# Kernel tuning notes

Hardware: AMD Instinct MI355X
Metric: run time of the kernel (lower is better)

## Reference

```python
import jax, jax.numpy as jnp
import numpy as np

B, N, D, H = 128, 32768, 768, 16
DH = D // H          # per-head hidden_size = memory_dim // num_heads = 48
BETA = 0.25          # scaling (inverse temperature)
STEPS = 5            # update_steps_max
TOPK = 4


def _ln(x, g, b):
    # torch nn.LayerNorm over last dim (biased variance, eps=1e-5), affine
    m = jnp.mean(x, axis=-1, keepdims=True)
    v = jnp.var(x, axis=-1, keepdims=True)
    return (x - m) * jax.lax.rsqrt(v + 1e-5) * g + b


def _l2norm(x):
    # F.normalize(x, dim=-1): x / max(||x||, 1e-12)
    n = jnp.linalg.norm(x, axis=-1, keepdims=True)
    return x / jnp.maximum(n, 1e-12)


def setup_inputs() -> dict:
    key = jax.random.key(0)
    ks = jax.random.split(key, 8)
    s = 0.05  # weight init scale to keep activations sane
    return {
        "query_embedding": jax.random.normal(ks[0], (B, D), jnp.float32),
        "memory_bank": jax.random.normal(ks[1], (N, D), jnp.float32),
        "ln_k_g": jnp.ones((D,), jnp.float32), "ln_k_b": jnp.zeros((D,), jnp.float32),
        "ln_q_g": jnp.ones((D,), jnp.float32), "ln_q_b": jnp.zeros((D,), jnp.float32),
        "ln_v_g": jnp.ones((D,), jnp.float32), "ln_v_b": jnp.zeros((D,), jnp.float32),
        "Wq": jax.random.normal(ks[2], (D, D), jnp.float32) * s, "bq": jnp.zeros((D,), jnp.float32),
        "Wk": jax.random.normal(ks[3], (D, D), jnp.float32) * s, "bk": jnp.zeros((D,), jnp.float32),
        "Wv": jax.random.normal(ks[4], (D, D), jnp.float32) * s, "bv": jnp.zeros((D,), jnp.float32),
        "Wo": jax.random.normal(ks[5], (D, D), jnp.float32) * s, "bo": jnp.zeros((D,), jnp.float32),
        "W1": jax.random.normal(ks[6], (D, D), jnp.float32) * s, "b1": jnp.zeros((D,), jnp.float32),
        "W2": jax.random.normal(ks[7], (D, D), jnp.float32) * s, "b2": jnp.zeros((D,), jnp.float32),
    }


def reference(query_embedding, memory_bank, ln_k_g, ln_k_b, ln_q_g, ln_q_b,
              ln_v_g, ln_v_b, Wq, bq, Wk, bk, Wv, bv, Wo, bo, W1, b1, W2, b2):
    # Affine LayerNorms on stored pattern, state pattern, pattern projection.
    # memory_bank is shared across the batch, so normalize/project it ONCE
    # instead of materializing the (B, N, D) expand from the torch code.
    stored = _ln(memory_bank, ln_k_g, ln_k_b)        # (N, D)
    state = _ln(query_embedding, ln_q_g, ln_q_b)     # (B, D) -- state pattern, seq len 1
    projp = _ln(memory_bank, ln_v_g, ln_v_b)         # (N, D)

    k = (stored @ Wk.T + bk).reshape(N, H, DH)       # (N, H, dh)
    v = (projp @ Wv.T + bv).reshape(N, H, DH)        # (N, H, dh)
    q = (state @ Wq.T + bq).reshape(B, H, DH)        # (B, H, dh)

    # Hopfield convergence: xi <- softmax(beta * xi K^T) K, repeated STEPS times
    def step(xi, _):
        attn = jax.nn.softmax(BETA * jnp.einsum('bhd,nhd->bhn', xi, k), axis=-1)
        return jnp.einsum('bhn,nhd->bhd', attn, k), None

    xi, _ = jax.lax.scan(step, q, None, length=STEPS)

    # Final readout against the (separately normalized) pattern projection V
    attn = jax.nn.softmax(BETA * jnp.einsum('bhd,nhd->bhn', xi, k), axis=-1)  # (B, H, N)
    converged = jnp.einsum('bhn,nhd->bhd', attn, v).reshape(B, D) @ Wo.T + bo  # (B, D)

    # Retrieval head: residual + MLP + cosine-sim logits + top-k
    combined = query_embedding + converged
    rq = jax.nn.relu(combined @ W1.T + b1) @ W2.T + b2
    logits = (_l2norm(rq) @ _l2norm(memory_bank).T) * 20.0   # (B, N)
    top_indices = jax.lax.top_k(logits, TOPK)[1]              # (B, TOPK)
    return top_indices, logits
```

## Files before the change

kernel.cpp:

```cpp
#include <hip/hip_runtime.h>
#include <math.h>

#define NTOT 32768
#define DMODEL 768
#define BSZ 128
#define NHEAD 16
#define DH 48
#define BETA 0.25f

typedef _Float16 f16;
typedef f16 f16x8 __attribute__((ext_vector_type(8)));
typedef f16 f16x4 __attribute__((ext_vector_type(4)));
typedef float f32x4 __attribute__((ext_vector_type(4)));

__global__ __launch_bounds__(256)
void row_stats(const float* __restrict__ X, int M, float* __restrict__ mean,
               float* __restrict__ rstd, float* __restrict__ l2inv) {
  const int row = blockIdx.x * 4 + (threadIdx.x >> 6);
  const int lane = threadIdx.x & 63;
  if (row >= M) return;
  const float* x = X + (size_t)row * DMODEL;
  float s = 0.f, s2 = 0.f;
  for (int i = lane; i < DMODEL; i += 64) {
    float v = x[i];
    s += v; s2 += v * v;
  }
#pragma unroll
  for (int off = 32; off; off >>= 1) {
    s  += __shfl_xor(s, off);
    s2 += __shfl_xor(s2, off);
  }
  if (lane == 0) {
    float mu = s * (1.f / DMODEL);
    float var = s2 * (1.f / DMODEL) - mu * mu;
    mean[row] = mu;
    rstd[row] = rsqrtf(var + 1e-5f);
    if (l2inv) l2inv[row] = 1.f / fmaxf(sqrtf(s2), 1e-12f);
  }
}

__global__ __launch_bounds__(256)
void prep_w(const float* __restrict__ Wk, const float* __restrict__ bk,
            const float* __restrict__ gk, const float* __restrict__ blnk,
            const float* __restrict__ Wv, const float* __restrict__ bv,
            const float* __restrict__ gv, const float* __restrict__ blnv,
            f16* __restrict__ Wc_hi, f16* __restrict__ Wc_lo,
            float* __restrict__ biasc) {
  const int o = blockIdx.x * 4 + (threadIdx.x >> 6);
  const int lane = threadIdx.x & 63;
  const bool isK = o < DMODEL;
  const float* W = isK ? (Wk + (size_t)o * DMODEL)
                       : (Wv + (size_t)(o - DMODEL) * DMODEL);
  const float* g   = isK ? gk : gv;
  const float* bln = isK ? blnk : blnv;
  float bacc = 0.f;
  for (int d = lane * 4; d < DMODEL; d += 256) {
    const float4 wv = *(const float4*)(W + d);
    const float4 g4 = *(const float4*)(g + d);
    const float4 b4 = *(const float4*)(bln + d);
    bacc += wv.x * b4.x + wv.y * b4.y + wv.z * b4.z + wv.w * b4.w;
    const float sv[4] = {wv.x * g4.x * 16.f, wv.y * g4.y * 16.f,
                         wv.z * g4.z * 16.f, wv.w * g4.w * 16.f};
    f16x4 h4, l4;
#pragma unroll
    for (int j = 0; j < 4; j++) {
      const f16 h = (f16)sv[j];
      h4[j] = h;
      l4[j] = (f16)(sv[j] - (float)h);
    }
    *(f16x4*)(Wc_hi + (size_t)o * DMODEL + d) = h4;
    *(f16x4*)(Wc_lo + (size_t)o * DMODEL + d) = l4;
  }
#pragma unroll
  for (int off = 32; off; off >>= 1) bacc += __shfl_xor(bacc, off);
  if (lane == 0) biasc[o] = (isK ? bk[o] : bv[o - DMODEL]) + bacc;
}

__global__ __launch_bounds__(256)
void proj_dual_mfma(const float* __restrict__ mb, const float* __restrict__ mean,
                    const float* __restrict__ rstd,
                    const f16* __restrict__ Wc_hi, const f16* __restrict__ Wc_lo,
                    const float* __restrict__ biasc,
                    f16* __restrict__ k_hi, f16* __restrict__ k_lo,
                    f16* __restrict__ v_hi, f16* __restrict__ v_lo) {
  __shared__ __align__(16) f16 As[2][128][40];
  __shared__ __align__(16) f16 Bs[2][128][40];
  const int t = threadIdx.x;
  const int n0 = blockIdx.x * 128;
  const int m0 = blockIdx.y * 128;
  const int w = t >> 6, lane = t & 63;
  const int l15 = lane & 15, lq = lane >> 4;
  const int wm = w >> 1, wn = w & 1;
  const int sr = t >> 1, sh = t & 1;
  const float mu = mean[m0 + sr];
  const float rs = rstd[m0 + sr];

  f32x4 acc[4][4];
#pragma unroll
  for (int a = 0; a < 4; a++)
#pragma unroll
    for (int b = 0; b < 4; b++)
#pragma unroll
      for (int r = 0; r < 4; r++) acc[a][b][r] = 0.f;

  for (int k0 = 0; k0 < DMODEL; k0 += 32) {
    __syncthreads();
    {
      const float* ap = mb + (size_t)(m0 + sr) * DMODEL + k0 + sh * 16;
      float x[16];
#pragma unroll
      for (int c = 0; c < 4; c++) {
        const float4 v4 = *(const float4*)(ap + c * 4);
        x[c * 4 + 0] = v4.x; x[c * 4 + 1] = v4.y;
        x[c * 4 + 2] = v4.z; x[c * 4 + 3] = v4.w;
      }
      f16x8 h0, h1, l0, l1;
#pragma unroll
      for (int j = 0; j < 8; j++) {
        const float s = (x[j] - mu) * rs;
        const f16 h = (f16)s;
        h0[j] = h; l0[j] = (f16)(s - (float)h);
      }
#pragma unroll
      for (int j = 0; j < 8; j++) {
        const float s = (x[8 + j] - mu) * rs;
        const f16 h = (f16)s;
        h1[j] = h; l1[j] = (f16)(s - (float)h);
      }
      *(f16x8*)&As[0][sr][sh * 16] = h0;
      *(f16x8*)&As[0][sr][sh * 16 + 8] = h1;
      *(f16x8*)&As[1][sr][sh * 16] = l0;
      *(f16x8*)&As[1][sr][sh * 16 + 8] = l1;
    }
    {
      const size_t boff = (size_t)(n0 + sr) * DMODEL + k0 + sh * 16;
      f16x8 bh0 = *(const f16x8*)(Wc_hi + boff);
      f16x8 bh1 = *(const f16x8*)(Wc_hi + boff + 8);
      f16x8 bl0 = *(const f16x8*)(Wc_lo + boff);
      f16x8 bl1 = *(const f16x8*)(Wc_lo + boff + 8);
      *(f16x8*)&Bs[0][sr][sh * 16] = bh0;
      *(f16x8*)&Bs[0][sr][sh * 16 + 8] = bh1;
      *(f16x8*)&Bs[1][sr][sh * 16] = bl0;
      *(f16x8*)&Bs[1][sr][sh * 16 + 8] = bl1;
    }
    __syncthreads();
    f16x8 nhh[4], nhl[4];
#pragma unroll
    for (int fm = 0; fm < 4; fm++) {
      const int row = wm * 64 + fm * 16 + l15;
      nhh[fm] = *(const f16x8*)&As[0][row][lq * 8];
      nhl[fm] = *(const f16x8*)&As[1][row][lq * 8];
    }
    f16x8 wh[4], wl[4];
#pragma unroll
    for (int fo = 0; fo < 4; fo++) {
      const int row = wn * 64 + fo * 16 + l15;
      wh[fo] = *(const f16x8*)&Bs[0][row][lq * 8];
      wl[fo] = *(const f16x8*)&Bs[1][row][lq * 8];
    }
#pragma unroll
    for (int fo = 0; fo < 4; fo++)
#pragma unroll
      for (int fm = 0; fm < 4; fm++) {
        f32x4 a = acc[fo][fm];
        a = __builtin_amdgcn_mfma_f32_16x16x32_f16(wh[fo], nhh[fm], a, 0, 0, 0);
        a = __builtin_amdgcn_mfma_f32_16x16x32_f16(wh[fo], nhl[fm], a, 0, 0, 0);
        a = __builtin_amdgcn_mfma_f32_16x16x32_f16(wl[fo], nhh[fm], a, 0, 0, 0);
        acc[fo][fm] = a;
      }
  }
  const int oc = n0 + wn * 64;
  const bool isK = oc < DMODEL;
  f16* oh = isK ? k_hi : v_hi;
  f16* ol = isK ? k_lo : v_lo;
  const int obase = (isK ? oc : oc - DMODEL) + lq * 4;
#pragma unroll
  for (int fo = 0; fo < 4; fo++) {
    const float4 bb = *(const float4*)(biasc + oc + fo * 16 + lq * 4);
    const float bbv[4] = {bb.x, bb.y, bb.z, bb.w};
    const int o = obase + fo * 16;
#pragma unroll
    for (int fm = 0; fm < 4; fm++) {
      const size_t moff = (size_t)(m0 + wm * 64 + fm * 16 + l15) * DMODEL + o;
      f16x4 h4, l4;
#pragma unroll
      for (int r = 0; r < 4; r++) {
        const float v = acc[fo][fm][r] * 0.0625f + bbv[r];
        const f16 h = (f16)v;
        h4[r] = h;
        l4[r] = (f16)(v - (float)h);
      }
      *(f16x4*)(oh + moff) = h4;
      *(f16x4*)(ol + moff) = l4;
    }
  }
}

__global__ __launch_bounds__(256)
void ln_gemm_f32(const float* __restrict__ A, const float* __restrict__ mean,
                 const float* __restrict__ rstd, const float* __restrict__ g,
                 const float* __restrict__ bln, const float* __restrict__ W,
                 const float* __restrict__ bias, float* __restrict__ out) {
  __shared__ float As[16][68];
  __shared__ float Ws[16][68];
  const int t = threadIdx.x;
  const int m0 = blockIdx.y << 6, n0 = blockIdx.x << 6;
  const int tm = t >> 4, tn = t & 15;
  const int lr = t >> 2;
  const int lk = (t & 3) << 2;
  const float muL = mean[m0 + lr];
  const float rsL = rstd[m0 + lr];
  float acc[4][4] = {};
  for (int k0 = 0; k0 < DMODEL; k0 += 16) {
    float4 a4 = *(const float4*)(A + (size_t)(m0 + lr) * DMODEL + k0 + lk);
    float4 g4 = *(const float4*)(g + k0 + lk);
    float4 b4 = *(const float4*)(bln + k0 + lk);
    As[lk + 0][lr] = (a4.x - muL) * rsL * g4.x + b4.x;
    As[lk + 1][lr] = (a4.y - muL) * rsL * g4.y + b4.y;
    As[lk + 2][lr] = (a4.z - muL) * rsL * g4.z + b4.z;
    As[lk + 3][lr] = (a4.w - muL) * rsL * g4.w + b4.w;
    float4 w4 = *(const float4*)(W + (size_t)(n0 + lr) * DMODEL + k0 + lk);
    Ws[lk + 0][lr] = w4.x;
    Ws[lk + 1][lr] = w4.y;
    Ws[lk + 2][lr] = w4.z;
    Ws[lk + 3][lr] = w4.w;
    __syncthreads();
#pragma unroll
    for (int kk = 0; kk < 16; kk++) {
      const float4 av = *(const float4*)(&As[kk][tm * 4]);
      const float4 bv = *(const float4*)(&Ws[kk][tn * 4]);
      const float a[4] = {av.x, av.y, av.z, av.w};
      const float b[4] = {bv.x, bv.y, bv.z, bv.w};
#pragma unroll
      for (int i = 0; i < 4; i++)
#pragma unroll
        for (int j = 0; j < 4; j++) acc[i][j] += a[i] * b[j];
    }
    __syncthreads();
  }
  const float4 bia = *(const float4*)(bias + n0 + tn * 4);
  const float bb[4] = {bia.x, bia.y, bia.z, bia.w};
#pragma unroll
  for (int i = 0; i < 4; i++) {
    const int m = m0 + tm * 4 + i;
    float4 o4;
    o4.x = acc[i][0] + bb[0];
    o4.y = acc[i][1] + bb[1];
    o4.z = acc[i][2] + bb[2];
    o4.w = acc[i][3] + bb[3];
    *(float4*)(out + (size_t)m * DMODEL + n0 + tn * 4) = o4;
  }
}

__global__ __launch_bounds__(256)
void gemm_bias(const float* __restrict__ A, const float* __restrict__ W,
               const float* __restrict__ bias, const float* __restrict__ add,
               float* __restrict__ out, int relu) {
  __shared__ float As[16][68];
  __shared__ float Ws[16][68];
  const int t = threadIdx.x;
  const int m0 = blockIdx.y << 6, n0 = blockIdx.x << 6;
  const int tm = t >> 4, tn = t & 15;
  const int lr = t >> 2;
  const int lk = (t & 3) << 2;
  float acc[4][4] = {};
  for (int k0 = 0; k0 < DMODEL; k0 += 16) {
    float4 a4 = *(const float4*)(A + (size_t)(m0 + lr) * DMODEL + k0 + lk);
    As[lk + 0][lr] = a4.x;
    As[lk + 1][lr] = a4.y;
    As[lk + 2][lr] = a4.z;
    As[lk + 3][lr] = a4.w;
    float4 w4 = *(const float4*)(W + (size_t)(n0 + lr) * DMODEL + k0 + lk);
    Ws[lk + 0][lr] = w4.x;
    Ws[lk + 1][lr] = w4.y;
    Ws[lk + 2][lr] = w4.z;
    Ws[lk + 3][lr] = w4.w;
    __syncthreads();
#pragma unroll
    for (int kk = 0; kk < 16; kk++) {
      const float4 av = *(const float4*)(&As[kk][tm * 4]);
      const float4 bv = *(const float4*)(&Ws[kk][tn * 4]);
      const float a[4] = {av.x, av.y, av.z, av.w};
      const float b[4] = {bv.x, bv.y, bv.z, bv.w};
#pragma unroll
      for (int i = 0; i < 4; i++)
#pragma unroll
        for (int j = 0; j < 4; j++) acc[i][j] += a[i] * b[j];
    }
    __syncthreads();
  }
  const float4 bia = *(const float4*)(bias + n0 + tn * 4);
  const float bb[4] = {bia.x, bia.y, bia.z, bia.w};
#pragma unroll
  for (int i = 0; i < 4; i++) {
    const int m = m0 + tm * 4 + i;
    float v[4];
#pragma unroll
    for (int j = 0; j < 4; j++) v[j] = acc[i][j] + bb[j];
    if (add) {
      const float4 a4 = *(const float4*)(add + (size_t)m * DMODEL + n0 + tn * 4);
      v[0] += a4.x; v[1] += a4.y; v[2] += a4.z; v[3] += a4.w;
    }
    if (relu) {
#pragma unroll
      for (int j = 0; j < 4; j++) v[j] = fmaxf(v[j], 0.f);
    }
    float4 o4 = {v[0], v[1], v[2], v[3]};
    *(float4*)(out + (size_t)m * DMODEL + n0 + tn * 4) = o4;
  }
}

__global__ __launch_bounds__(256)
void logits_gemm(const float* __restrict__ A, const float* __restrict__ Bm,
                 const float* __restrict__ ainv, const float* __restrict__ binv,
                 float* __restrict__ out) {
  __shared__ float As[16][68];
  __shared__ float Ws[16][68];
  const int t = threadIdx.x;
  const int m0 = blockIdx.y << 6, n0 = blockIdx.x << 6;
  const int tm = t >> 4, tn = t & 15;
  const int lr = t >> 2;
  const int lk = (t & 3) << 2;
  float acc[4][4] = {};
  for (int k0 = 0; k0 < DMODEL; k0 += 16) {
    float4 a4 = *(const float4*)(A + (size_t)(m0 + lr) * DMODEL + k0 + lk);
    As[lk + 0][lr] = a4.x;
    As[lk + 1][lr] = a4.y;
    As[lk + 2][lr] = a4.z;
    As[lk + 3][lr] = a4.w;
    float4 w4 = *(const float4*)(Bm + (size_t)(n0 + lr) * DMODEL + k0 + lk);
    Ws[lk + 0][lr] = w4.x;
    Ws[lk + 1][lr] = w4.y;
    Ws[lk + 2][lr] = w4.z;
    Ws[lk + 3][lr] = w4.w;
    __syncthreads();
#pragma unroll
    for (int kk = 0; kk < 16; kk++) {
      const float4 av = *(const float4*)(&As[kk][tm * 4]);
      const float4 bv = *(const float4*)(&Ws[kk][tn * 4]);
      const float a[4] = {av.x, av.y, av.z, av.w};
      const float b[4] = {bv.x, bv.y, bv.z, bv.w};
#pragma unroll
      for (int i = 0; i < 4; i++)
#pragma unroll
        for (int j = 0; j < 4; j++) acc[i][j] += a[i] * b[j];
    }
    __syncthreads();
  }
  const float4 bi4 = *(const float4*)(binv + n0 + tn * 4);
  const float bi[4] = {bi4.x, bi4.y, bi4.z, bi4.w};
#pragma unroll
  for (int i = 0; i < 4; i++) {
    const int m = m0 + tm * 4 + i;
    const float sa = 20.f * ainv[m];
    float4 o4;
    o4.x = acc[i][0] * sa * bi[0];
    o4.y = acc[i][1] * sa * bi[1];
    o4.z = acc[i][2] * sa * bi[2];
    o4.w = acc[i][3] * sa * bi[3];
    *(float4*)(out + (size_t)m * NTOT + n0 + tn * 4) = o4;
  }
}

__global__ __launch_bounds__(256)
void split_xi_k(const float* __restrict__ xi, f16* __restrict__ hi,
                f16* __restrict__ lo) {
  const int i = blockIdx.x * 256 + threadIdx.x;
  float4 v = ((const float4*)xi)[i];
  float s[4] = {v.x * BETA, v.y * BETA, v.z * BETA, v.w * BETA};
  f16x4 h4, l4;
#pragma unroll
  for (int j = 0; j < 4; j++) {
    f16 h = (f16)s[j];
    h4[j] = h;
    l4[j] = (f16)(s[j] - (float)h);
  }
  ((f16x4*)hi)[i] = h4;
  ((f16x4*)lo)[i] = l4;
}

#define FCHUNK 64
#define FROWS (NTOT / FCHUNK)

__global__ __launch_bounds__(256)
void flash_round(const f16* __restrict__ k_hi, const f16* __restrict__ k_lo,
                 const f16* __restrict__ val_hi, const f16* __restrict__ val_lo,
                 const f16* __restrict__ xi_hi, const f16* __restrict__ xi_lo,
                 float* __restrict__ part_ml, float* __restrict__ part_o) {
  const int h = blockIdx.y, chunk = blockIdx.x;
  const int tid = threadIdx.x, w = tid >> 6, lane = tid & 63;
  const int l15 = lane & 15, lq = lane >> 4;
  const int b0 = w * 32;

  __shared__ __align__(16) f16 krow[2][32][56];
  __shared__ __align__(16) f16 vT[2][48][40];
  __shared__ __align__(16) f16 pHi[4][32][40];
  __shared__ __align__(16) f16 pLo[4][32][40];

  const f16x8 zf = {};
  f16x8 xqh[2][2], xql[2][2];
#pragma unroll
  for (int bt = 0; bt < 2; bt++) {
    const size_t xoff = (size_t)(b0 + bt * 16 + l15) * DMODEL + h * DH;
    xqh[bt][0] = *(const f16x8*)(xi_hi + xoff + lq * 8);
    xql[bt][0] = *(const f16x8*)(xi_lo + xoff + lq * 8);
    const size_t xo1 = xoff + 32 + (lq & 1) * 8;
    f16x8 th = *(const f16x8*)(xi_hi + xo1);
    f16x8 tl = *(const f16x8*)(xi_lo + xo1);
    xqh[bt][1] = (lq < 2) ? th : zf;
    xql[bt][1] = (lq < 2) ? tl : zf;
  }

  float m[2] = {-1e30f, -1e30f}, lsum[2] = {0.f, 0.f};
  f32x4 O[3][2];
#pragma unroll
  for (int mt = 0; mt < 3; mt++)
#pragma unroll
    for (int bt = 0; bt < 2; bt++)
#pragma unroll
      for (int j = 0; j < 4; j++) O[mt][bt][j] = 0.f;

  const int nbase = chunk * FROWS;
  for (int it = 0; it < FROWS / 32; it++) {
    const int gn0 = nbase + it * 32;
    __syncthreads();
    for (int j = tid; j < 384; j += 256) {
      const int tsel = j / 192;
      const int q = j - tsel * 192;
      const int r = q / 6;
      const int d0 = (q - r * 6) * 8;
      const size_t goff = (size_t)(gn0 + r) * DMODEL + h * DH + d0;
      const f16* kp = (tsel ? k_lo : k_hi) + goff;
      const f16* vp = (tsel ? val_lo : val_hi) + goff;
      f16x8 kv = *(const f16x8*)kp;
      f16x8 vv = *(const f16x8*)vp;
      *(f16x8*)&krow[tsel][r][d0] = kv;
#pragma unroll
      for (int jj = 0; jj < 8; jj++) vT[tsel][d0 + jj][r] = vv[jj];
    }
    __syncthreads();

    f16x8 akh[2][2], akl[2][2];
#pragma unroll
    for (int nt = 0; nt < 2; nt++) {
      const int row = nt * 16 + l15;
      akh[nt][0] = *(const f16x8*)&krow[0][row][lq * 8];
      akl[nt][0] = *(const f16x8*)&krow[1][row][lq * 8];
      f16x8 t0 = *(const f16x8*)&krow[0][row][32 + (lq & 1) * 8];
      f16x8 t1 = *(const f16x8*)&krow[1][row][32 + (lq & 1) * 8];
      akh[nt][1] = (lq < 2) ? t0 : zf;
      akl[nt][1] = (lq < 2) ? t1 : zf;
    }
    f32x4 S[2][2];
#pragma unroll
    for (int nt = 0; nt < 2; nt++)
#pragma unroll
      for (int bt = 0; bt < 2; bt++) {
        f32x4 s = {};
        s = __builtin_amdgcn_mfma_f32_16x16x32_f16(akh[nt][0], xqh[bt][0], s, 0, 0, 0);
        s = __builtin_amdgcn_mfma_f32_16x16x32_f16(akh[nt][1], xqh[bt][1], s, 0, 0, 0);
        s = __builtin_amdgcn_mfma_f32_16x16x32_f16(akh[nt][0], xql[bt][0], s, 0, 0, 0);
        s = __builtin_amdgcn_mfma_f32_16x16x32_f16(akh[nt][1], xql[bt][1], s, 0, 0, 0);
        s = __builtin_amdgcn_mfma_f32_16x16x32_f16(akl[nt][0], xqh[bt][0], s, 0, 0, 0);
        s = __builtin_amdgcn_mfma_f32_16x16x32_f16(akl[nt][1], xqh[bt][1], s, 0, 0, 0);
        S[nt][bt] = s;
      }
    float sc[2];
#pragma unroll
    for (int bt = 0; bt < 2; bt++) {
      float mx = S[0][bt][0];
#pragma unroll
      for (int r = 1; r < 4; r++) mx = fmaxf(mx, S[0][bt][r]);
#pragma unroll
      for (int r = 0; r < 4; r++) mx = fmaxf(mx, S[1][bt][r]);
      mx = fmaxf(mx, __shfl_xor(mx, 16));
      mx = fmaxf(mx, __shfl_xor(mx, 32));
      const float mnew = fmaxf(m[bt], mx);
      sc[bt] = __expf(m[bt] - mnew);
      float ps = 0.f;
#pragma unroll
      for (int nt = 0; nt < 2; nt++) {
        f16x4 ph, pl;
#pragma unroll
        for (int r = 0; r < 4; r++) {
          const float p = __expf(S[nt][bt][r] - mnew);
          ps += p;
          const f16 hh = (f16)p;
          ph[r] = hh;
          pl[r] = (f16)(p - (float)hh);
        }
        *(f16x4*)&pHi[w][bt * 16 + l15][nt * 16 + lq * 4] = ph;
        *(f16x4*)&pLo[w][bt * 16 + l15][nt * 16 + lq * 4] = pl;
      }
      ps += __shfl_xor(ps, 16);
      ps += __shfl_xor(ps, 32);
      lsum[bt] = lsum[bt] * sc[bt] + ps;
      m[bt] = mnew;
    }
    __asm__ volatile("s_waitcnt lgkmcnt(0)" ::: "memory");
    f16x8 avh[3], avl[3];
#pragma unroll
    for (int mt = 0; mt < 3; mt++) {
      avh[mt] = *(const f16x8*)&vT[0][mt * 16 + l15][lq * 8];
      avl[mt] = *(const f16x8*)&vT[1][mt * 16 + l15][lq * 8];
    }
    f16x8 pbh[2], pbl[2];
#pragma unroll
    for (int bt = 0; bt < 2; bt++) {
      pbh[bt] = *(const f16x8*)&pHi[w][bt * 16 + l15][lq * 8];
      pbl[bt] = *(const f16x8*)&pLo[w][bt * 16 + l15][lq * 8];
    }
#pragma unroll
    for (int mt = 0; mt < 3; mt++)
#pragma unroll
      for (int bt = 0; bt < 2; bt++) {
#pragma unroll
        for (int j = 0; j < 4; j++) O[mt][bt][j] *= sc[bt];
        f32x4 o = O[mt][bt];
        o = __builtin_amdgcn_mfma_f32_16x16x32_f16(avh[mt], pbh[bt], o, 0, 0, 0);
        o = __builtin_amdgcn_mfma_f32_16x16x32_f16(avh[mt], pbl[bt], o, 0, 0, 0);
        o = __builtin_amdgcn_mfma_f32_16x16x32_f16(avl[mt], pbh[bt], o, 0, 0, 0);
        O[mt][bt] = o;
      }
  }
  const int pc = h * FCHUNK + chunk;
  if (lq == 0) {
#pragma unroll
    for (int bt = 0; bt < 2; bt++) {
      float* pm = part_ml + ((size_t)pc * BSZ + b0 + bt * 16 + l15) * 2;
      pm[0] = m[bt];
      pm[1] = lsum[bt];
    }
  }
#pragma unroll
  for (int mt = 0; mt < 3; mt++)
#pragma unroll
    for (int bt = 0; bt < 2; bt++) {
      float* po = part_o + ((size_t)pc * BSZ + b0 + bt * 16 + l15) * 48 +
                  mt * 16 + lq * 4;
      *(f32x4*)po = O[mt][bt];
    }
}

__global__ __launch_bounds__(64)
void hopfield_combine(const float* __restrict__ part_ml,
                      const float* __restrict__ part_o, float* __restrict__ dst) {
  const int bh = blockIdx.x;
  const int h = bh >> 7, b = bh & 127;
  const int c = threadIdx.x;
  __shared__ float w[64];
  const float* pm = part_ml + ((size_t)(h * 64 + c) * BSZ + b) * 2;
  const float mp = pm[0];
  const float lp = pm[1];
  float M = mp;
#pragma unroll
  for (int off = 32; off; off >>= 1) M = fmaxf(M, __shfl_xor(M, off));
  const float wp = __expf(mp - M);
  w[c] = wp;
  float L = lp * wp;
#pragma unroll
  for (int off = 32; off; off >>= 1) L += __shfl_xor(L, off);
  __syncthreads();
  if (c < DH) {
    float o = 0.f;
    for (int p = 0; p < 64; p++)
      o += part_o[((size_t)(h * 64 + p) * BSZ + b) * 48 + c] * w[p];
    dst[(size_t)b * DMODEL + h * DH + c] = o / L;
  }
}

__global__ __launch_bounds__(256)
void topk_kernel(const float* __restrict__ logits, float* __restrict__ outIdx) {
  const int b = blockIdx.x;
  const int t = threadIdx.x;
  const float* row = logits + (size_t)b * NTOT;
  float v[4] = {-1e30f, -1e30f, -1e30f, -1e30f};
  int id[4] = {0x7fffffff, 0x7fffffff, 0x7fffffff, 0x7fffffff};
  for (int n = t; n < NTOT; n += 256) {
    const float x = row[n];
    if (x > v[3]) {
      v[3] = x; id[3] = n;
#pragma unroll
      for (int s = 3; s > 0; s--) {
        const bool sw = (v[s] > v[s - 1]) || (v[s] == v[s - 1] && id[s] < id[s - 1]);
        if (sw) {
          float tv = v[s]; v[s] = v[s - 1]; v[s - 1] = tv;
          int ti = id[s]; id[s] = id[s - 1]; id[s - 1] = ti;
        }
      }
    }
  }
  __shared__ float sv[256][4];
  __shared__ int si[256][4];
#pragma unroll
  for (int j = 0; j < 4; j++) { sv[t][j] = v[j]; si[t][j] = id[j]; }
  for (int str = 128; str >= 1; str >>= 1) {
    __syncthreads();
    if (t < str) {
      float a[4], c[4];
      int ai[4], ci[4];
#pragma unroll
      for (int j = 0; j < 4; j++) {
        a[j] = sv[t][j]; ai[j] = si[t][j];
        c[j] = sv[t + str][j]; ci[j] = si[t + str][j];
      }
      float rv[4]; int ri[4];
      int p = 0, q = 0;
#pragma unroll
      for (int oo = 0; oo < 4; oo++) {
        const bool ta = (a[p] > c[q]) || (a[p] == c[q] && ai[p] < ci[q]);
        if (ta) { rv[oo] = a[p]; ri[oo] = ai[p]; p++; }
        else    { rv[oo] = c[q]; ri[oo] = ci[q]; q++; }
      }
#pragma unroll
      for (int j = 0; j < 4; j++) { sv[t][j] = rv[j]; si[t][j] = ri[j]; }
    }
  }
  if (t == 0) {
#pragma unroll
    for (int j = 0; j < 4; j++) outIdx[b * 4 + j] = (float)si[0][j];
  }
}

extern "C" void kernel_launch(void* const* d_in, const int* in_sizes, int n_in,
                              void* d_out, int out_size, void* d_ws, size_t ws_size,
                              hipStream_t stream) {
  const float* qe    = (const float*)d_in[0];
  const float* mb    = (const float*)d_in[1];
  const float* ln_kg = (const float*)d_in[2];
  const float* ln_kb = (const float*)d_in[3];
  const float* ln_qg = (const float*)d_in[4];
  const float* ln_qb = (const float*)d_in[5];
  const float* ln_vg = (const float*)d_in[6];
  const float* ln_vb = (const float*)d_in[7];
  const float* Wq = (const float*)d_in[8];
  const float* bq = (const float*)d_in[9];
  const float* Wk = (const float*)d_in[10];
  const float* bk = (const float*)d_in[11];
  const float* Wv = (const float*)d_in[12];
  const float* bv = (const float*)d_in[13];
  const float* Wo = (const float*)d_in[14];
  const float* bo = (const float*)d_in[15];
  const float* W1 = (const float*)d_in[16];
  const float* b1 = (const float*)d_in[17];
  const float* W2 = (const float*)d_in[18];
  const float* b2 = (const float*)d_in[19];

  float* out = (float*)d_out;
  float* logits = out + BSZ * 4;

  float* ws = (float*)d_ws;
  size_t off = 0;
  auto alloc = [&](size_t n) { float* p = ws + off; off += n; return p; };
  const size_t ND2 = (size_t)NTOT * DMODEL / 2;
  float* mb_mean = alloc(NTOT);
  float* mb_rstd = alloc(NTOT);
  float* mb_l2i  = alloc(NTOT);
  float* q_mean  = alloc(128);
  float* q_rstd  = alloc(128);
  float* rq_inv  = alloc(128);
  float* pad_    = alloc(384);
  f16* k_hi = (f16*)alloc(ND2);
  f16* k_lo = (f16*)alloc(ND2);
  f16* v_hi = (f16*)alloc(ND2);
  f16* v_lo = (f16*)alloc(ND2);
  float* part_ml = alloc((size_t)NHEAD * FCHUNK * BSZ * 2);
  float* part_o  = alloc((size_t)NHEAD * FCHUNK * BSZ * 48);
  float* xi   = alloc((size_t)BSZ * DMODEL);
  float* conv = alloc((size_t)BSZ * DMODEL);
  float* comb = alloc((size_t)BSZ * DMODEL);
  float* h1   = alloc((size_t)BSZ * DMODEL);
  f16* xi_hi = (f16*)alloc((size_t)BSZ * DMODEL / 2);
  f16* xi_lo = (f16*)alloc((size_t)BSZ * DMODEL / 2);
  f16* Wc_hi = (f16*)alloc((size_t)2 * DMODEL * DMODEL / 2);
  f16* Wc_lo = (f16*)alloc((size_t)2 * DMODEL * DMODEL / 2);
  float* biasc = alloc(2 * DMODEL);
  (void)ws_size; (void)in_sizes; (void)n_in; (void)out_size; (void)pad_;

  row_stats<<<NTOT / 4, 256, 0, stream>>>(mb, NTOT, mb_mean, mb_rstd, mb_l2i);
  row_stats<<<BSZ / 4, 256, 0, stream>>>(qe, BSZ, q_mean, q_rstd, nullptr);
  prep_w<<<2 * DMODEL / 4, 256, 0, stream>>>(Wk, bk, ln_kg, ln_kb,
                                             Wv, bv, ln_vg, ln_vb,
                                             Wc_hi, Wc_lo, biasc);

  proj_dual_mfma<<<dim3(2 * DMODEL / 128, NTOT / 128), 256, 0, stream>>>(
      mb, mb_mean, mb_rstd, Wc_hi, Wc_lo, biasc, k_hi, k_lo, v_hi, v_lo);
  ln_gemm_f32<<<dim3(DMODEL / 64, BSZ / 64), 256, 0, stream>>>(
      qe, q_mean, q_rstd, ln_qg, ln_qb, Wq, bq, xi);

  for (int r = 0; r < 6; r++) {
    const f16* valHi = (r == 5) ? v_hi : k_hi;
    const f16* valLo = (r == 5) ? v_lo : k_lo;
    float* dst = (r == 5) ? conv : xi;
    split_xi_k<<<96, 256, 0, stream>>>(xi, xi_hi, xi_lo);
    flash_round<<<dim3(FCHUNK, NHEAD), 256, 0, stream>>>(
        k_hi, k_lo, valHi, valLo, xi_hi, xi_lo, part_ml, part_o);
    hopfield_combine<<<BSZ * NHEAD, 64, 0, stream>>>(part_ml, part_o, dst);
  }

  gemm_bias<<<dim3(DMODEL / 64, BSZ / 64), 256, 0, stream>>>(conv, Wo, bo, qe, comb, 0);
  gemm_bias<<<dim3(DMODEL / 64, BSZ / 64), 256, 0, stream>>>(comb, W1, b1, nullptr, h1, 1);
  float* rq = conv;
  gemm_bias<<<dim3(DMODEL / 64, BSZ / 64), 256, 0, stream>>>(h1, W2, b2, nullptr, rq, 0);

  row_stats<<<BSZ / 4, 256, 0, stream>>>(rq, BSZ, q_mean, q_rstd, rq_inv);
  logits_gemm<<<dim3(NTOT / 64, BSZ / 64), 256, 0, stream>>>(rq, mb, rq_inv, mb_l2i, logits);

  topk_kernel<<<BSZ, 256, 0, stream>>>(logits, out);
}
```

Measured before the change: 1.474 ms.

## Move logits GEMM to split-f16 MFMA and pre-split LN inputs for projection

Replaces the scalar fp32 logits GEMM with a split hi/lo f16 MFMA kernel. The memory bank and rq are first converted to hi/lo f16, and the memory bank's split copy reuses the k buffers once they are no longer needed. The projection GEMM now reads LayerNorm'd, pre-split f16 inputs produced by a separate pass when the workspace is large enough, instead of normalizing and splitting inside the GEMM. The flash round also skips the duplicate value load when values equal keys. Costs are extra full-bank conversion passes and workspace aliasing, and the three-term split product loses a little precision compared with fp32.

After: 1.505 ms. 1.02x slower.

```diff
diff --git a/kernel.cpp b/kernel.cpp
--- a/kernel.cpp
+++ b/kernel.cpp
@@ -37,6 +37,48 @@
     rstd[row] = rsqrtf(var + 1e-5f);
     if (l2inv) l2inv[row] = 1.f / fmaxf(sqrtf(s2), 1e-12f);
   }
+}
+
+__global__ __launch_bounds__(256)
+void split_ln(const float* __restrict__ X, const float* __restrict__ mean,
+              const float* __restrict__ rstd, f16* __restrict__ hi,
+              f16* __restrict__ lo) {
+  const int i8 = blockIdx.x * 256 + threadIdx.x;
+  const int row = i8 / 96;
+  const float mu = mean[row], rs = rstd[row];
+  const float* xp = X + (size_t)i8 * 8;
+  const float4 a = *(const float4*)xp;
+  const float4 b = *(const float4*)(xp + 4);
+  const float x[8] = {a.x, a.y, a.z, a.w, b.x, b.y, b.z, b.w};
+  f16x8 h, l;
+#pragma unroll
+  for (int j = 0; j < 8; j++) {
+    const float s = (x[j] - mu) * rs;
+    const f16 hv = (f16)s;
+    h[j] = hv;
+    l[j] = (f16)(s - (float)hv);
+  }
+  *(f16x8*)(hi + (size_t)i8 * 8) = h;
+  *(f16x8*)(lo + (size_t)i8 * 8) = l;
+}
+
+__global__ __launch_bounds__(256)
+void split_plain(const float* __restrict__ X, f16* __restrict__ hi,
+                 f16* __restrict__ lo) {
+  const int i8 = blockIdx.x * 256 + threadIdx.x;
+  const float* xp = X + (size_t)i8 * 8;
+  const float4 a = *(const float4*)xp;
+  const float4 b = *(const float4*)(xp + 4);
+  const float x[8] = {a.x, a.y, a.z, a.w, b.x, b.y, b.z, b.w};
+  f16x8 h, l;
+#pragma unroll
+  for (int j = 0; j < 8; j++) {
+    const f16 hv = (f16)x[j];
+    h[j] = hv;
+    l[j] = (f16)(x[j] - (float)hv);
+  }
+  *(f16x8*)(hi + (size_t)i8 * 8) = h;
+  *(f16x8*)(lo + (size_t)i8 * 8) = l;
 }
 
 __global__ __launch_bounds__(256)
@@ -77,12 +119,113 @@
 }
 
 __global__ __launch_bounds__(256)
-void proj_dual_mfma(const float* __restrict__ mb, const float* __restrict__ mean,
-                    const float* __restrict__ rstd,
-                    const f16* __restrict__ Wc_hi, const f16* __restrict__ Wc_lo,
-                    const float* __restrict__ biasc,
-                    f16* __restrict__ k_hi, f16* __restrict__ k_lo,
-                    f16* __restrict__ v_hi, f16* __restrict__ v_lo) {
+void proj_dual_v2(const f16* __restrict__ nh_hi, const f16* __restrict__ nh_lo,
+                  const f16* __restrict__ Wc_hi, const f16* __restrict__ Wc_lo,
+                  const float* __restrict__ biasc,
+                  f16* __restrict__ k_hi, f16* __restrict__ k_lo,
+                  f16* __restrict__ v_hi, f16* __restrict__ v_lo) {
+  __shared__ __align__(16) f16 As[2][128][40];
+  __shared__ __align__(16) f16 Bs[2][128][40];
+  const int t = threadIdx.x;
+  const int n0 = blockIdx.x * 128;
+  const int m0 = blockIdx.y * 128;
+  const int w = t >> 6, lane = t & 63;
+  const int l15 = lane & 15, lq = lane >> 4;
+  const int wm = w >> 1, wn = w & 1;
+  const int sr = t >> 1, sh = t & 1;
+
+  f32x4 acc[4][4];
+#pragma unroll
+  for (int a = 0; a < 4; a++)
+#pragma unroll
+    for (int b = 0; b < 4; b++)
+#pragma unroll
+      for (int r = 0; r < 4; r++) acc[a][b][r] = 0.f;
+
+  for (int k0 = 0; k0 < DMODEL; k0 += 32) {
+    __syncthreads();
+    {
+      const size_t aoff = (size_t)(m0 + sr) * DMODEL + k0 + sh * 16;
+      f16x8 ah0 = *(const f16x8*)(nh_hi + aoff);
+      f16x8 ah1 = *(const f16x8*)(nh_hi + aoff + 8);
+      f16x8 al0 = *(const f16x8*)(nh_lo + aoff);
+      f16x8 al1 = *(const f16x8*)(nh_lo + aoff + 8);
+      *(f16x8*)&As[0][sr][sh * 16] = ah0;
+      *(f16x8*)&As[0][sr][sh * 16 + 8] = ah1;
+      *(f16x8*)&As[1][sr][sh * 16] = al0;
+      *(f16x8*)&As[1][sr][sh * 16 + 8] = al1;
+    }
+    {
+      const size_t boff = (size_t)(n0 + sr) * DMODEL + k0 + sh * 16;
+      f16x8 bh0 = *(const f16x8*)(Wc_hi + boff);
+      f16x8 bh1 = *(const f16x8*)(Wc_hi + boff + 8);
+      f16x8 bl0 = *(const f16x8*)(Wc_lo + boff);
+      f16x8 bl1 = *(const f16x8*)(Wc_lo + boff + 8);
+      *(f16x8*)&Bs[0][sr][sh * 16] = bh0;
+      *(f16x8*)&Bs[0][sr][sh * 16 + 8] = bh1;
+      *(f16x8*)&Bs[1][sr][sh * 16] = bl0;
+      *(f16x8*)&Bs[1][sr][sh * 16 + 8] = bl1;
+    }
+    __syncthreads();
+    f16x8 nhh[4], nhl[4];
+#pragma unroll
+    for (int fm = 0; fm < 4; fm++) {
+      const int row = wm * 64 + fm * 16 + l15;
+      nhh[fm] = *(const f16x8*)&As[0][row][lq * 8];
+      nhl[fm] = *(const f16x8*)&As[1][row][lq * 8];
+    }
+    f16x8 wh[4], wl[4];
+#pragma unroll
+    for (int fo = 0; fo < 4; fo++) {
+      const int row = wn * 64 + fo * 16 + l15;
+      wh[fo] = *(const f16x8*)&Bs[0][row][lq * 8];
+      wl[fo] = *(const f16x8*)&Bs[1][row][lq * 8];
+    }
+#pragma unroll
+    for (int fo = 0; fo < 4; fo++)
+#pragma unroll
+      for (int fm = 0; fm < 4; fm++) {
+        f32x4 a = acc[fo][fm];
+        a = __builtin_amdgcn_mfma_f32_16x16x32_f16(wh[fo], nhh[fm], a, 0, 0, 0);
+        a = __builtin_amdgcn_mfma_f32_16x16x32_f16(wh[fo], nhl[fm], a, 0, 0, 0);
+        a = __builtin_amdgcn_mfma_f32_16x16x32_f16(wl[fo], nhh[fm], a, 0, 0, 0);
+        acc[fo][fm] = a;
+      }
+  }
+  const int oc = n0 + wn * 64;
+  const bool isK = oc < DMODEL;
+  f16* oh = isK ? k_hi : v_hi;
+  f16* ol = isK ? k_lo : v_lo;
+  const int obase = (isK ? oc : oc - DMODEL) + lq * 4;
+#pragma unroll
+  for (int fo = 0; fo < 4; fo++) {
+    const float4 bb = *(const float4*)(biasc + oc + fo * 16 + lq * 4);
+    const float bbv[4] = {bb.x, bb.y, bb.z, bb.w};
+    const int o = obase + fo * 16;
+#pragma unroll
+    for (int fm = 0; fm < 4; fm++) {
+      const size_t moff = (size_t)(m0 + wm * 64 + fm * 16 + l15) * DMODEL + o;
+      f16x4 h4, l4;
+#pragma unroll
+      for (int r = 0; r < 4; r++) {
+        const float v = acc[fo][fm][r] * 0.0625f + bbv[r];
+        const f16 h = (f16)v;
+        h4[r] = h;
+        l4[r] = (f16)(v - (float)h);
+      }
+      *(f16x4*)(oh + moff) = h4;
+      *(f16x4*)(ol + moff) = l4;
+    }
+  }
+}
+
+__global__ __launch_bounds__(256)
+void proj_dual_insplit(const float* __restrict__ mb, const float* __restrict__ mean,
+                       const float* __restrict__ rstd,
+                       const f16* __restrict__ Wc_hi, const f16* __restrict__ Wc_lo,
+                       const float* __restrict__ biasc,
+                       f16* __restrict__ k_hi, f16* __restrict__ k_lo,
+                       f16* __restrict__ v_hi, f16* __restrict__ v_lo) {
   __shared__ __align__(16) f16 As[2][128][40];
   __shared__ __align__(16) f16 Bs[2][128][40];
   const int t = threadIdx.x;
@@ -94,7 +237,6 @@
   const int sr = t >> 1, sh = t & 1;
   const float mu = mean[m0 + sr];
   const float rs = rstd[m0 + sr];
-
   f32x4 acc[4][4];
 #pragma unroll
   for (int a = 0; a < 4; a++)
@@ -102,7 +244,6 @@
     for (int b = 0; b < 4; b++)
 #pragma unroll
       for (int r = 0; r < 4; r++) acc[a][b][r] = 0.f;
-
   for (int k0 = 0; k0 < DMODEL; k0 += 32) {
     __syncthreads();
     {
@@ -192,6 +333,95 @@
       }
       *(f16x4*)(oh + moff) = h4;
       *(f16x4*)(ol + moff) = l4;
+    }
+  }
+}
+
+__global__ __launch_bounds__(256)
+void logits_mfma(const f16* __restrict__ mb_hi, const f16* __restrict__ mb_lo,
+                 const f16* __restrict__ rq_hi, const f16* __restrict__ rq_lo,
+                 const float* __restrict__ ainv, const float* __restrict__ binv,
+                 float* __restrict__ out) {
+  __shared__ __align__(16) f16 As[2][128][40];
+  __shared__ __align__(16) f16 Bs[2][128][40];
+  const int t = threadIdx.x;
+  const int n0 = blockIdx.x * 128;
+  const int w = t >> 6, lane = t & 63;
+  const int l15 = lane & 15, lq = lane >> 4;
+  const int wb = w >> 1, wn = w & 1;
+  const int sr = t >> 1, sh = t & 1;
+
+  f32x4 acc[4][4];
+#pragma unroll
+  for (int a = 0; a < 4; a++)
+#pragma unroll
+    for (int b = 0; b < 4; b++)
+#pragma unroll
+      for (int r = 0; r < 4; r++) acc[a][b][r] = 0.f;
+
+  for (int k0 = 0; k0 < DMODEL; k0 += 32) {
+    __syncthreads();
+    {
+      const size_t aoff = (size_t)(n0 + sr) * DMODEL + k0 + sh * 16;
+      f16x8 ah0 = *(const f16x8*)(mb_hi + aoff);
+      f16x8 ah1 = *(const f16x8*)(mb_hi + aoff + 8);
+      f16x8 al0 = *(const f16x8*)(mb_lo + aoff);
+      f16x8 al1 = *(const f16x8*)(mb_lo + aoff + 8);
+      *(f16x8*)&As[0][sr][sh * 16] = ah0;
+      *(f16x8*)&As[0][sr][sh * 16 + 8] = ah1;
+      *(f16x8*)&As[1][sr][sh * 16] = al0;
+      *(f16x8*)&As[1][sr][sh * 16 + 8] = al1;
+    }
+    {
+      const size_t boff = (size_t)sr * DMODEL + k0 + sh * 16;
+      f16x8 bh0 = *(const f16x8*)(rq_hi + boff);
+      f16x8 bh1 = *(const f16x8*)(rq_hi + boff + 8);
+      f16x8 bl0 = *(const f16x8*)(rq_lo + boff);
+      f16x8 bl1 = *(const f16x8*)(rq_lo + boff + 8);
+      *(f16x8*)&Bs[0][sr][sh * 16] = bh0;
+      *(f16x8*)&Bs[0][sr][sh * 16 + 8] = bh1;
+      *(f16x8*)&Bs[1][sr][sh * 16] = bl0;
+      *(f16x8*)&Bs[1][sr][sh * 16 + 8] = bl1;
+    }
+    __syncthreads();
+    f16x8 ah[4], al[4];
+#pragma unroll
+    for (int fn = 0; fn < 4; fn++) {
+      const int row = wn * 64 + fn * 16 + l15;
+      ah[fn] = *(const f16x8*)&As[0][row][lq * 8];
+      al[fn] = *(const f16x8*)&As[1][row][lq * 8];
+    }
+    f16x8 bh[4], bl[4];
+#pragma unroll
+    for (int fb = 0; fb < 4; fb++) {
+      const int row = wb * 64 + fb * 16 + l15;
+      bh[fb] = *(const f16x8*)&Bs[0][row][lq * 8];
+      bl[fb] = *(const f16x8*)&Bs[1][row][lq * 8];
+    }
+#pragma unroll
+    for (int fn = 0; fn < 4; fn++)
+#pragma unroll
+      for (int fb = 0; fb < 4; fb++) {
+        f32x4 a = acc[fn][fb];
+        a = __builtin_amdgcn_mfma_f32_16x16x32_f16(ah[fn], bh[fb], a, 0, 0, 0);
+        a = __builtin_amdgcn_mfma_f32_16x16x32_f16(ah[fn], bl[fb], a, 0, 0, 0);
+        a = __builtin_amdgcn_mfma_f32_16x16x32_f16(al[fn], bh[fb], a, 0, 0, 0);
+        acc[fn][fb] = a;
+      }
+  }
+#pragma unroll
+  for (int fn = 0; fn < 4; fn++) {
+    const int gn = n0 + wn * 64 + fn * 16 + lq * 4;
+    const float4 bi4 = *(const float4*)(binv + gn);
+    const float bi[4] = {bi4.x, bi4.y, bi4.z, bi4.w};
+#pragma unroll
+    for (int fb = 0; fb < 4; fb++) {
+      const int b = wb * 64 + fb * 16 + l15;
+      const float sa = 20.f * ainv[b];
+      f32x4 o;
+#pragma unroll
+      for (int r = 0; r < 4; r++) o[r] = acc[fn][fb][r] * sa * bi[r];
+      *(f32x4*)(out + (size_t)b * NTOT + gn) = o;
     }
   }
 }
@@ -311,58 +541,6 @@
 }
 
 __global__ __launch_bounds__(256)
-void logits_gemm(const float* __restrict__ A, const float* __restrict__ Bm,
-                 const float* __restrict__ ainv, const float* __restrict__ binv,
-                 float* __restrict__ out) {
-  __shared__ float As[16][68];
-  __shared__ float Ws[16][68];
-  const int t = threadIdx.x;
-  const int m0 = blockIdx.y << 6, n0 = blockIdx.x << 6;
-  const int tm = t >> 4, tn = t & 15;
-  const int lr = t >> 2;
-  const int lk = (t & 3) << 2;
-  float acc[4][4] = {};
-  for (int k0 = 0; k0 < DMODEL; k0 += 16) {
-    float4 a4 = *(const float4*)(A + (size_t)(m0 + lr) * DMODEL + k0 + lk);
-    As[lk + 0][lr] = a4.x;
-    As[lk + 1][lr] = a4.y;
-    As[lk + 2][lr] = a4.z;
-    As[lk + 3][lr] = a4.w;
-    float4 w4 = *(const float4*)(Bm + (size_t)(n0 + lr) * DMODEL + k0 + lk);
-    Ws[lk + 0][lr] = w4.x;
-    Ws[lk + 1][lr] = w4.y;
-    Ws[lk + 2][lr] = w4.z;
-    Ws[lk + 3][lr] = w4.w;
-    __syncthreads();
-#pragma unroll
-    for (int kk = 0; kk < 16; kk++) {
-      const float4 av = *(const float4*)(&As[kk][tm * 4]);
-      const float4 bv = *(const float4*)(&Ws[kk][tn * 4]);
-      const float a[4] = {av.x, av.y, av.z, av.w};
-      const float b[4] = {bv.x, bv.y, bv.z, bv.w};
-#pragma unroll
-      for (int i = 0; i < 4; i++)
-#pragma unroll
-        for (int j = 0; j < 4; j++) acc[i][j] += a[i] * b[j];
-    }
-    __syncthreads();
-  }
-  const float4 bi4 = *(const float4*)(binv + n0 + tn * 4);
-  const float bi[4] = {bi4.x, bi4.y, bi4.z, bi4.w};
-#pragma unroll
-  for (int i = 0; i < 4; i++) {
-    const int m = m0 + tm * 4 + i;
-    const float sa = 20.f * ainv[m];
-    float4 o4;
-    o4.x = acc[i][0] * sa * bi[0];
-    o4.y = acc[i][1] * sa * bi[1];
-    o4.z = acc[i][2] * sa * bi[2];
-    o4.w = acc[i][3] * sa * bi[3];
-    *(float4*)(out + (size_t)m * NTOT + n0 + tn * 4) = o4;
-  }
-}
-
-__global__ __launch_bounds__(256)
 void split_xi_k(const float* __restrict__ xi, f16* __restrict__ hi,
                 f16* __restrict__ lo) {
   const int i = blockIdx.x * 256 + threadIdx.x;
@@ -386,7 +564,8 @@
 void flash_round(const f16* __restrict__ k_hi, const f16* __restrict__ k_lo,
                  const f16* __restrict__ val_hi, const f16* __restrict__ val_lo,
                  const f16* __restrict__ xi_hi, const f16* __restrict__ xi_lo,
-                 float* __restrict__ part_ml, float* __restrict__ part_o) {
+                 float* __restrict__ part_ml, float* __restrict__ part_o,
+                 int valIsK) {
   const int h = blockIdx.y, chunk = blockIdx.x;
   const int tid = threadIdx.x, w = tid >> 6, lane = tid & 63;
   const int l15 = lane & 15, lq = lane >> 4;
@@ -431,9 +610,14 @@
       const int d0 = (q - r * 6) * 8;
       const size_t goff = (size_t)(gn0 + r) * DMODEL + h * DH + d0;
       const f16* kp = (tsel ? k_lo : k_hi) + goff;
-      const f16* vp = (tsel ? val_lo : val_hi) + goff;
       f16x8 kv = *(const f16x8*)kp;
-      f16x8 vv = *(const f16x8*)vp;
+      f16x8 vv;
+      if (valIsK) {
+        vv = kv;
+      } else {
+        const f16* vp = (tsel ? val_lo : val_hi) + goff;
+        vv = *(const f16x8*)vp;
+      }
       *(f16x8*)&krow[tsel][r][d0] = kv;
 #pragma unroll
       for (int jj = 0; jj < 8; jj++) vT[tsel][d0 + jj][r] = vv[jj];
@@ -649,10 +833,17 @@
   float* out = (float*)d_out;
   float* logits = out + BSZ * 4;
 
+  const size_t ND16 = (size_t)NTOT * DMODEL / 2;
+  const size_t PART = (size_t)NHEAD * FCHUNK * BSZ * (2 + 48);
+  const size_t fixed = 3 * NTOT + 768 + 4 * ND16 + 4 * (size_t)BSZ * DMODEL +
+                       4 * (size_t)BSZ * DMODEL / 2 +
+                       2 * (size_t)2 * DMODEL * DMODEL / 2 + 2 * DMODEL;
+  const bool fast = (fixed + 2 * ND16) * sizeof(float) <= ws_size;
+  const size_t nhpart = fast ? 2 * ND16 : PART;
+
   float* ws = (float*)d_ws;
   size_t off = 0;
   auto alloc = [&](size_t n) { float* p = ws + off; off += n; return p; };
-  const size_t ND2 = (size_t)NTOT * DMODEL / 2;
   float* mb_mean = alloc(NTOT);
   float* mb_rstd = alloc(NTOT);
   float* mb_l2i  = alloc(NTOT);
@@ -660,22 +851,29 @@
   float* q_rstd  = alloc(128);
   float* rq_inv  = alloc(128);
   float* pad_    = alloc(384);
-  f16* k_hi = (f16*)alloc(ND2);
-  f16* k_lo = (f16*)alloc(ND2);
-  f16* v_hi = (f16*)alloc(ND2);
-  f16* v_lo = (f16*)alloc(ND2);
-  float* part_ml = alloc((size_t)NHEAD * FCHUNK * BSZ * 2);
-  float* part_o  = alloc((size_t)NHEAD * FCHUNK * BSZ * 48);
+  f16* k_hi = (f16*)alloc(ND16);
+  f16* k_lo = (f16*)alloc(ND16);
+  f16* v_hi = (f16*)alloc(ND16);
+  f16* v_lo = (f16*)alloc(ND16);
+  float* nhpart_base = alloc(nhpart);
+  f16* nh_hi = (f16*)nhpart_base;
+  f16* nh_lo = (f16*)(nhpart_base + ND16);
+  float* part_ml = nhpart_base;
+  float* part_o  = nhpart_base + (size_t)NHEAD * FCHUNK * BSZ * 2;
   float* xi   = alloc((size_t)BSZ * DMODEL);
   float* conv = alloc((size_t)BSZ * DMODEL);
   float* comb = alloc((size_t)BSZ * DMODEL);
   float* h1   = alloc((size_t)BSZ * DMODEL);
   f16* xi_hi = (f16*)alloc((size_t)BSZ * DMODEL / 2);
   f16* xi_lo = (f16*)alloc((size_t)BSZ * DMODEL / 2);
+  f16* rq_hi = (f16*)alloc((size_t)BSZ * DMODEL / 2);
+  f16* rq_lo = (f16*)alloc((size_t)BSZ * DMODEL / 2);
   f16* Wc_hi = (f16*)alloc((size_t)2 * DMODEL * DMODEL / 2);
   f16* Wc_lo = (f16*)alloc((size_t)2 * DMODEL * DMODEL / 2);
   float* biasc = alloc(2 * DMODEL);
-  (void)ws_size; (void)in_sizes; (void)n_in; (void)out_size; (void)pad_;
+  f16* mb16_hi = (f16*)k_hi;
+  f16* mb16_lo = (f16*)k_lo;
+  (void)in_sizes; (void)n_in; (void)out_size; (void)pad_;
 
   row_stats<<<NTOT / 4, 256, 0, stream>>>(mb, NTOT, mb_mean, mb_rstd, mb_l2i);
   row_stats<<<BSZ / 4, 256, 0, stream>>>(qe, BSZ, q_mean, q_rstd, nullptr);
@@ -683,18 +881,26 @@
                                              Wv, bv, ln_vg, ln_vb,
                                              Wc_hi, Wc_lo, biasc);
 
-  proj_dual_mfma<<<dim3(2 * DMODEL / 128, NTOT / 128), 256, 0, stream>>>(
-      mb, mb_mean, mb_rstd, Wc_hi, Wc_lo, biasc, k_hi, k_lo, v_hi, v_lo);
+  if (fast) {
+    split_ln<<<(NTOT * DMODEL / 8) / 256, 256, 0, stream>>>(
+        mb, mb_mean, mb_rstd, nh_hi, nh_lo);
+    proj_dual_v2<<<dim3(2 * DMODEL / 128, NTOT / 128), 256, 0, stream>>>(
+        nh_hi, nh_lo, Wc_hi, Wc_lo, biasc, k_hi, k_lo, v_hi, v_lo);
+  } else {
+    proj_dual_insplit<<<dim3(2 * DMODEL / 128, NTOT / 128), 256, 0, stream>>>(
+        mb, mb_mean, mb_rstd, Wc_hi, Wc_lo, biasc, k_hi, k_lo, v_hi, v_lo);
+  }
   ln_gemm_f32<<<dim3(DMODEL / 64, BSZ / 64), 256, 0, stream>>>(
       qe, q_mean, q_rstd, ln_qg, ln_qb, Wq, bq, xi);
 
   for (int r = 0; r < 6; r++) {
-    const f16* valHi = (r == 5) ? v_hi : k_hi;
-    const f16* valLo = (r == 5) ? v_lo : k_lo;
+    const int valIsK = (r != 5);
+    const f16* valHi = valIsK ? k_hi : v_hi;
+    const f16* valLo = valIsK ? k_lo : v_lo;
     float* dst = (r == 5) ? conv : xi;
     split_xi_k<<<96, 256, 0, stream>>>(xi, xi_hi, xi_lo);
     flash_round<<<dim3(FCHUNK, NHEAD), 256, 0, stream>>>(
-        k_hi, k_lo, valHi, valLo, xi_hi, xi_lo, part_ml, part_o);
+        k_hi, k_lo, valHi, valLo, xi_hi, xi_lo, part_ml, part_o, valIsK);
     hopfield_combine<<<BSZ * NHEAD, 64, 0, stream>>>(part_ml, part_o, dst);
   }
 
@@ -704,7 +910,10 @@
   gemm_bias<<<dim3(DMODEL / 64, BSZ / 64), 256, 0, stream>>>(h1, W2, b2, nullptr, rq, 0);
 
   row_stats<<<BSZ / 4, 256, 0, stream>>>(rq, BSZ, q_mean, q_rstd, rq_inv);
-  logits_gemm<<<dim3(NTOT / 64, BSZ / 64), 256, 0, stream>>>(rq, mb, rq_inv, mb_l2i, logits);
+  split_plain<<<(NTOT * DMODEL / 8) / 256, 256, 0, stream>>>(mb, mb16_hi, mb16_lo);
+  split_plain<<<(BSZ * DMODEL / 8) / 256, 256, 0, stream>>>(rq, rq_hi, rq_lo);
+  logits_mfma<<<NTOT / 128, 256, 0, stream>>>(mb16_hi, mb16_lo, rq_hi, rq_lo,
+                                              rq_inv, mb_l2i, logits);
 
   topk_kernel<<<BSZ, 256, 0, stream>>>(logits, out);
 }
```
